# Kernel optimization log

Hardware: AMD Instinct MI355X
Metric: run time of the kernel (lower is better)

The kernel has to match this reference:

```python
import jax, jax.numpy as jnp
import numpy as np

N = 100000
E = 2000000
K = 3


def setup_inputs() -> dict:
    key = jax.random.key(0)
    ks = jax.random.split(key, 6)
    x = jax.random.normal(ks[0], (N, 1), jnp.float32)
    edge_index = jax.random.randint(ks[1], (2, E), 0, N, dtype=jnp.int64)
    W1 = jax.random.normal(ks[2], (K, 1, 32), jnp.float32) * 0.5
    b1 = jnp.zeros((32,), jnp.float32)
    W2 = jax.random.normal(ks[3], (K, 32, 32), jnp.float32) * (1.0 / np.sqrt(32.0))
    b2 = jnp.zeros((32,), jnp.float32)
    Wfc = jax.random.normal(ks[4], (32, 1), jnp.float32) * (1.0 / np.sqrt(32.0))
    bfc = jnp.zeros((1,), jnp.float32)
    return dict(x=x, edge_index=edge_index, W1=W1, b1=b1, W2=W2, b2=b2, Wfc=Wfc, bfc=bfc)


def _cheb_norm(edge_index, n):
    # PyG ChebConv.__norm__ with normalization='sym', lambda_max=2.0:
    # L = I - D^{-1/2} A D^{-1/2}; L_hat = (2/lmax)*L - I = -D^{-1/2} A D^{-1/2} (zero diag)
    src, dst = edge_index[0], edge_index[1]
    w = jnp.ones((edge_index.shape[1],), jnp.float32)
    deg = jax.ops.segment_sum(w, src, num_segments=n)
    dinv = jnp.where(deg > 0, jax.lax.rsqrt(jnp.maximum(deg, 1.0)), 0.0)
    norm = -dinv[src] * w * dinv[dst]
    return src, dst, norm


def _propagate(x, src, dst, norm, n):
    # y[i] = sum_{e: dst[e]=i} norm[e] * x[src[e]]  (gather-scatter SpMM)
    return jax.ops.segment_sum(norm[:, None] * x[src], dst, num_segments=n)


def _cheb_conv(x, src, dst, norm, W, b, n):
    Tx0 = x
    out = Tx0 @ W[0]
    Tx1 = _propagate(Tx0, src, dst, norm, n)
    out = out + Tx1 @ W[1]
    for k in range(2, W.shape[0]):  # small fixed K, structurally distinct weights
        Tx2 = 2.0 * _propagate(Tx1, src, dst, norm, n) - Tx0
        out = out + Tx2 @ W[k]
        Tx0, Tx1 = Tx1, Tx2
    return out + b


def reference(x, edge_index, W1, b1, W2, b2, Wfc, bfc):
    n = x.shape[0]
    src, dst, norm = _cheb_norm(edge_index, n)
    h = jax.nn.relu(_cheb_conv(x, src, dst, norm, W1, b1, n))
    h = jax.nn.relu(_cheb_conv(h, src, dst, norm, W2, b2, n))
    return h @ Wfc + bfc
```

## Files before the change

kernel.cpp:

```cpp
#include <hip/hip_runtime.h>
#include <hip/hip_fp16.h>


#define BS 256
#define NC 32
#define NRH 16
#define NRB 16
#define HB 1024
#define RCAP 6250

__global__ __launch_bounds__(HB) void k_hist32(const int* __restrict__ src,
                                               const int* __restrict__ dst,
                                               int* __restrict__ deg32,
                                               int* __restrict__ cnt32,
                                               int n, int E, int ce) {
    __shared__ int hcnt[RCAP];
    __shared__ int hdeg[RCAP];
    int b = blockIdx.x, c = b & (NC - 1), r = b >> 5;
    int t = threadIdx.x;
    const int R = (n + NRH - 1) / NRH;
    int lo = r * R, hi = min(lo + R, n), len = hi - lo;
    for (int q = t; q < len; q += HB) { hcnt[q] = 0; hdeg[q] = 0; }
    __syncthreads();
    int e0 = c * ce, e1 = min(e0 + ce, E);
    if (e0 < e1) {
        const int4* d4 = reinterpret_cast<const int4*>(dst + e0);
        const int4* s4 = reinterpret_cast<const int4*>(src + e0);
        int L4 = (e1 - e0) >> 2;
        for (int m = 0; m * 4 * HB < L4; ++m) {
            int4 dv[4], sv[4];
            bool ok[4];
            #pragma unroll
            for (int q = 0; q < 4; ++q) {
                int idx = t + (m * 4 + q) * HB;
                ok[q] = idx < L4;
                if (ok[q]) { dv[q] = d4[idx]; sv[q] = s4[idx]; }
            }
            #pragma unroll
            for (int q = 0; q < 4; ++q) if (ok[q]) {
                int d;
                d = dv[q].x; if (d >= lo && d < hi) atomicAdd(&hcnt[d - lo], 1);
                d = dv[q].y; if (d >= lo && d < hi) atomicAdd(&hcnt[d - lo], 1);
                d = dv[q].z; if (d >= lo && d < hi) atomicAdd(&hcnt[d - lo], 1);
                d = dv[q].w; if (d >= lo && d < hi) atomicAdd(&hcnt[d - lo], 1);
                d = sv[q].x; if (d >= lo && d < hi) atomicAdd(&hdeg[d - lo], 1);
                d = sv[q].y; if (d >= lo && d < hi) atomicAdd(&hdeg[d - lo], 1);
                d = sv[q].z; if (d >= lo && d < hi) atomicAdd(&hdeg[d - lo], 1);
                d = sv[q].w; if (d >= lo && d < hi) atomicAdd(&hdeg[d - lo], 1);
            }
        }
        for (int e = e0 + ((e1 - e0) & ~3) + t; e < e1; e += HB) {
            int d = dst[e];
            if (d >= lo && d < hi) atomicAdd(&hcnt[d - lo], 1);
            int s = src[e];
            if (s >= lo && s < hi) atomicAdd(&hdeg[s - lo], 1);
        }
    }
    __syncthreads();
    int base = c * n + lo;
    for (int q = t; q < len; q += HB) {
        cnt32[base + q] = hcnt[q];
        deg32[base + q] = hdeg[q];
    }
}

__global__ void k_dinv32(const int* __restrict__ deg32, const int* __restrict__ cnt32,
                         const float* __restrict__ x, float* __restrict__ dinv,
                         float* __restrict__ u, float* __restrict__ w,
                         int* __restrict__ cnt, int n) {
    int i = blockIdx.x * BS + threadIdx.x;
    if (i < n) {
        int d = 0, ci = 0;
        #pragma unroll
        for (int c = 0; c < NC; ++c) { d += deg32[c * n + i]; ci += cnt32[c * n + i]; }
        float df = (float)d;
        float dv = (d > 0) ? rsqrtf(fmaxf(df, 1.0f)) : 0.0f;
        dinv[i] = dv;
        u[i] = dv * x[i];
        w[i] = -dv * dv;
        cnt[i] = ci;
    }
}

__global__ void k_scan2A(const int* __restrict__ cnt, int* __restrict__ rowptr,
                         int* __restrict__ part, int n) {
    __shared__ int sh[BS];
    int t = threadIdx.x, i = blockIdx.x * BS + t;
    int v = (i < n) ? cnt[i] : 0;
    sh[t] = v; __syncthreads();
    int acc = v;
    for (int d = 1; d < BS; d <<= 1) {
        int add = (t >= d) ? sh[t - d] : 0;
        __syncthreads();
        acc += add; sh[t] = acc;
        __syncthreads();
    }
    if (i < n) rowptr[i] = acc - v;
    if (t == BS - 1) part[blockIdx.x] = acc;
}

__global__ void k_scanB(int* __restrict__ part, int nb) {
    __shared__ int sh[512];
    int t = threadIdx.x;
    int v = (t < nb) ? part[t] : 0;
    sh[t] = v; __syncthreads();
    int acc = v;
    for (int d = 1; d < 512; d <<= 1) {
        int add = (t >= d) ? sh[t - d] : 0;
        __syncthreads();
        acc += add; sh[t] = acc;
        __syncthreads();
    }
    if (t < nb) part[t] = acc - v;
}

__global__ void k_scan2C(int* __restrict__ rowptr, const int* __restrict__ part, int n, int E) {
    int i = blockIdx.x * BS + threadIdx.x;
    if (i < n) rowptr[i] += part[i >> 8];
    if (i == n) rowptr[n] = E;
}

__global__ void k_frag(const int* __restrict__ cnt32, const int* __restrict__ rowptr,
                       int* __restrict__ cur32, int n) {
    int i = blockIdx.x * BS + threadIdx.x;
    if (i < n) {
        int run = rowptr[i];
        #pragma unroll
        for (int c = 0; c < NC; ++c) {
            cur32[c * n + i] = run;
            run += cnt32[c * n + i];
        }
    }
}

__global__ __launch_bounds__(HB) void k_build32(const int* __restrict__ src,
                                                const int* __restrict__ dst,
                                                const int* __restrict__ cur32,
                                                int* __restrict__ colv,
                                                int n, int E, int ce) {
    __shared__ int lcur[RCAP];
    int b = blockIdx.x, r = b & (NRB - 1), c = b >> 4;
    int t = threadIdx.x;
    const int R = (n + NRB - 1) / NRB;
    int lo = r * R, hi = min(lo + R, n), len = hi - lo;
    int base = c * n + lo;
    for (int q = t; q < len; q += HB) lcur[q] = cur32[base + q];
    __syncthreads();
    int e0 = c * ce, e1 = min(e0 + ce, E);
    if (e0 < e1) {
        const int4* d4 = reinterpret_cast<const int4*>(dst + e0);
        const int4* s4 = reinterpret_cast<const int4*>(src + e0);
        int L4 = (e1 - e0) >> 2;
        for (int m = 0; m * 4 * HB < L4; ++m) {
            int4 dv[4], sv[4];
            bool ok[4];
            #pragma unroll
            for (int q = 0; q < 4; ++q) {
                int idx = t + (m * 4 + q) * HB;
                ok[q] = idx < L4;
                if (ok[q]) { dv[q] = d4[idx]; sv[q] = s4[idx]; }
            }
            #pragma unroll
            for (int q = 0; q < 4; ++q) if (ok[q]) {
                int d;
                d = dv[q].x; if (d >= lo && d < hi) { int p = atomicAdd(&lcur[d - lo], 1); colv[p] = sv[q].x; }
                d = dv[q].y; if (d >= lo && d < hi) { int p = atomicAdd(&lcur[d - lo], 1); colv[p] = sv[q].y; }
                d = dv[q].z; if (d >= lo && d < hi) { int p = atomicAdd(&lcur[d - lo], 1); colv[p] = sv[q].z; }
                d = dv[q].w; if (d >= lo && d < hi) { int p = atomicAdd(&lcur[d - lo], 1); colv[p] = sv[q].w; }
            }
        }
        for (int e = e0 + ((e1 - e0) & ~3) + t; e < e1; e += HB) {
            int d = dst[e];
            if (d >= lo && d < hi) { int p = atomicAdd(&lcur[d - lo], 1); colv[p] = src[e]; }
        }
    }
}

__global__ void k_prop_s(const int* __restrict__ rowptr, const int* __restrict__ colv,
                         const float* __restrict__ in, float* __restrict__ g,
                         float* __restrict__ vout, const float* __restrict__ w, int n) {
    int i = blockIdx.x * BS + threadIdx.x;
    if (i >= n) return;
    int b = rowptr[i], e = rowptr[i + 1];
    float s = 0.0f;
    int j = b;
    for (; j + 4 <= e; j += 4) {
        int s0 = colv[j], s1 = colv[j + 1], s2 = colv[j + 2], s3 = colv[j + 3];
        float a0 = in[s0], a1 = in[s1], a2 = in[s2], a3 = in[s3];
        s += (a0 + a1) + (a2 + a3);
    }
    for (; j < e; ++j) s += in[colv[j]];
    g[i] = s;
    if (vout) vout[i] = w[i] * s;
}

__global__ void k_layer1(const float* __restrict__ x, const float* __restrict__ g1,
                         const float* __restrict__ g2, const float* __restrict__ dinv,
                         const float* __restrict__ W1, const float* __restrict__ b1,
                         float* __restrict__ h, __half* __restrict__ hs16, int n) {
    int idx = blockIdx.x * BS + threadIdx.x;
    if (idx < n * 32) {
        int i = idx >> 5, f = idx & 31;
        float x0 = x[i], dv = dinv[i];
        float t1 = -dv * g1[i];
        float t2 = -2.0f * dv * g2[i] - x0;
        float v = x0 * W1[f] + t1 * W1[32 + f] + t2 * W1[64 + f] + b1[f];
        v = fmaxf(v, 0.0f);
        h[idx] = v;
        hs16[idx] = __float2half_rn(dv * v);
    }
}

__global__ void k_prop_vh(const int* __restrict__ rowptr, const int* __restrict__ colv,
                          const __half* __restrict__ in16, const float* __restrict__ wsc,
                          float* __restrict__ outf, __half* __restrict__ out16, int n) {
    int t = blockIdx.x * BS + threadIdx.x;
    int node = t >> 3;
    if (node >= n) return;
    int ln4 = (t & 7) << 2;
    int b = rowptr[node], e = rowptr[node + 1];
    float4 acc = make_float4(0.f, 0.f, 0.f, 0.f);
    int j = b;
    for (; j + 8 <= e; j += 8) {
        int sx[8];
        #pragma unroll
        for (int q = 0; q < 8; ++q) sx[q] = colv[j + q];
        float2 raw[8];
        #pragma unroll
        for (int q = 0; q < 8; ++q)
            raw[q] = *reinterpret_cast<const float2*>(in16 + (size_t)sx[q] * 32 + ln4);
        #pragma unroll
        for (int q = 0; q < 8; ++q) {
            __half2 p0 = *reinterpret_cast<__half2*>(&raw[q].x);
            __half2 p1 = *reinterpret_cast<__half2*>(&raw[q].y);
            float2 a = __half22float2(p0), c = __half22float2(p1);
            acc.x += a.x; acc.y += a.y; acc.z += c.x; acc.w += c.y;
        }
    }
    for (; j < e; ++j) {
        int s = colv[j];
        float2 raw = *reinterpret_cast<const float2*>(in16 + (size_t)s * 32 + ln4);
        __half2 p0 = *reinterpret_cast<__half2*>(&raw.x);
        __half2 p1 = *reinterpret_cast<__half2*>(&raw.y);
        float2 a = __half22float2(p0), c = __half22float2(p1);
        acc.x += a.x; acc.y += a.y; acc.z += c.x; acc.w += c.y;
    }
    *reinterpret_cast<float4*>(outf + (size_t)node * 32 + ln4) = acc;
    float wn = wsc[node];
    __half2 o0 = __floats2half2_rn(wn * acc.x, wn * acc.y);
    __half2 o1 = __floats2half2_rn(wn * acc.z, wn * acc.w);
    float2 packed;
    *reinterpret_cast<__half2*>(&packed.x) = o0;
    *reinterpret_cast<__half2*>(&packed.y) = o1;
    *reinterpret_cast<float2*>(out16 + (size_t)node * 32 + ln4) = packed;
}

__global__ __launch_bounds__(BS) void k_prop_fc(
    const int* __restrict__ rowptr, const int* __restrict__ colv,
    const __half* __restrict__ gA16s, const float* __restrict__ h,
    const float* __restrict__ gA, const float* __restrict__ dinv,
    const float* __restrict__ W2, const float* __restrict__ b2,
    const float* __restrict__ Wfc, const float* __restrict__ bfc,
    float* __restrict__ out, int n) {
    __shared__ float W2s[3 * 32 * 32];
    int tid = threadIdx.x;
    for (int q = tid; q < 3 * 32 * 32; q += BS) W2s[q] = W2[q];
    __syncthreads();
    int nd = tid >> 3, ln = tid & 7, ln4 = ln << 2;
    int i = blockIdx.x * 32 + nd;
    if (i >= n) return;
    float4 acc = make_float4(0.f, 0.f, 0.f, 0.f);
    int b = rowptr[i], e = rowptr[i + 1];
    int j = b;
    for (; j + 8 <= e; j += 8) {
        int sx[8];
        #pragma unroll
        for (int q = 0; q < 8; ++q) sx[q] = colv[j + q];
        float2 raw[8];
        #pragma unroll
        for (int q = 0; q < 8; ++q)
            raw[q] = *reinterpret_cast<const float2*>(gA16s + (size_t)sx[q] * 32 + ln4);
        #pragma unroll
        for (int q = 0; q < 8; ++q) {
            __half2 p0 = *reinterpret_cast<__half2*>(&raw[q].x);
            __half2 p1 = *reinterpret_cast<__half2*>(&raw[q].y);
            float2 a = __half22float2(p0), c = __half22float2(p1);
            acc.x += a.x; acc.y += a.y; acc.z += c.x; acc.w += c.y;
        }
    }
    for (; j < e; ++j) {
        int s = colv[j];
        float2 raw = *reinterpret_cast<const float2*>(gA16s + (size_t)s * 32 + ln4);
        __half2 p0 = *reinterpret_cast<__half2*>(&raw.x);
        __half2 p1 = *reinterpret_cast<__half2*>(&raw.y);
        float2 a = __half22float2(p0), c = __half22float2(p1);
        acc.x += a.x; acc.y += a.y; acc.z += c.x; acc.w += c.y;
    }
    float dv = dinv[i];
    float4 hv  = *reinterpret_cast<const float4*>(h  + (size_t)i * 32 + ln4);
    float4 gav = *reinterpret_cast<const float4*>(gA + (size_t)i * 32 + ln4);
    float hkv[4] = { hv.x, hv.y, hv.z, hv.w };
    float s1v[4] = { -dv * gav.x, -dv * gav.y, -dv * gav.z, -dv * gav.w };
    float s2v[4] = { -2.0f * dv * acc.x - hv.x, -2.0f * dv * acc.y - hv.y,
                     -2.0f * dv * acc.z - hv.z, -2.0f * dv * acc.w - hv.w };
    float a0 = b2[ln4 + 0], a1 = b2[ln4 + 1], a2 = b2[ln4 + 2], a3 = b2[ln4 + 3];
    #pragma unroll
    for (int k = 0; k < 32; ++k) {
        int srcLn = k >> 2;
        float hk  = __shfl(hkv[k & 3], srcLn, 8);
        float s1k = __shfl(s1v[k & 3], srcLn, 8);
        float s2k = __shfl(s2v[k & 3], srcLn, 8);
        const float* w0 = W2s + k * 32 + ln4;
        a0 += hk * w0[0] + s1k * w0[1024] + s2k * w0[2048];
        a1 += hk * w0[1] + s1k * w0[1025] + s2k * w0[2049];
        a2 += hk * w0[2] + s1k * w0[1026] + s2k * w0[2050];
        a3 += hk * w0[3] + s1k * w0[1027] + s2k * w0[2051];
    }
    float p = fmaxf(a0, 0.f) * Wfc[ln4 + 0] + fmaxf(a1, 0.f) * Wfc[ln4 + 1]
            + fmaxf(a2, 0.f) * Wfc[ln4 + 2] + fmaxf(a3, 0.f) * Wfc[ln4 + 3];
    #pragma unroll
    for (int m = 4; m >= 1; m >>= 1) p += __shfl_xor(p, m, 8);
    if (ln == 0) out[i] = p + bfc[0];
}

extern "C" void kernel_launch(void* const* d_in, const int* in_sizes, int n_in,
                              void* d_out, int out_size, void* d_ws, size_t ws_size,
                              hipStream_t stream) {
    const float* x   = (const float*)d_in[0];
    const int*   ei  = (const int*)d_in[1];
    const float* W1  = (const float*)d_in[2];
    const float* b1  = (const float*)d_in[3];
    const float* W2  = (const float*)d_in[4];
    const float* b2  = (const float*)d_in[5];
    const float* Wfc = (const float*)d_in[6];
    const float* bfc = (const float*)d_in[7];
    float* out = (float*)d_out;

    const int n = in_sizes[0];
    const int E = in_sizes[1] / 2;
    const int* src = ei;
    const int* dst = ei + E;
    const int ce = (((E + NC - 1) / NC) + 3) & ~3;

    int*   cnt    = (int*)d_ws;
    int*   rowptr = cnt + n;
    int*   part   = rowptr + n + 4;
    float* dinv   = (float*)(part + 512);
    float* u      = dinv + n;
    float* w      = u + n;
    float* g1     = w + n;
    float* v1     = g1 + n;
    float* g2     = v1 + n;
    int*   colv   = (int*)(g2 + n);
    float* h      = (float*)(colv + E);
    float* R2     = h + (size_t)32 * n;
    float* gA     = R2 + (size_t)32 * n;
    __half* hs16  = (__half*)R2;
    __half* gA16s = (__half*)(R2 + (size_t)16 * n);
    int*   cnt32  = (int*)h;
    int*   cur32  = (int*)R2;
    int*   deg32  = (int*)gA;

    const int NB = (n + BS - 1) / BS;

    k_hist32<<<NC * NRH, HB, 0, stream>>>(src, dst, deg32, cnt32, n, E, ce);
    k_dinv32<<<NB, BS, 0, stream>>>(deg32, cnt32, x, dinv, u, w, cnt, n);
    k_scan2A<<<NB, BS, 0, stream>>>(cnt, rowptr, part, n);
    k_scanB<<<1, 512, 0, stream>>>(part, NB);
    k_scan2C<<<NB + 1, BS, 0, stream>>>(rowptr, part, n, E);
    k_frag<<<NB, BS, 0, stream>>>(cnt32, rowptr, cur32, n);
    k_build32<<<NC * NRB, HB, 0, stream>>>(src, dst, cur32, colv, n, E, ce);

    k_prop_s<<<NB, BS, 0, stream>>>(rowptr, colv, u, g1, v1, w, n);
    k_prop_s<<<NB, BS, 0, stream>>>(rowptr, colv, v1, g2, nullptr, nullptr, n);
    k_layer1<<<(n * 32 + BS - 1) / BS, BS, 0, stream>>>(x, g1, g2, dinv, W1, b1, h, hs16, n);

    k_prop_vh<<<(n * 8 + BS - 1) / BS, BS, 0, stream>>>(rowptr, colv, hs16, w, gA, gA16s, n);
    k_prop_fc<<<(n + 31) / 32, BS, 0, stream>>>(rowptr, colv, gA16s, h, gA, dinv,
                                                W2, b2, Wfc, bfc, out, n);
}
```

Before: 271.8 us.

## Use 4 lanes per node with 16-byte gathers and drop fp32 gA buffer

Both SpMM propagation kernels now assign 4 lanes per node instead of 8, and each lane gathers 8 halves with one 16-byte load, which halves the number of gather instructions per edge. k_prop_vh no longer writes the fp32 aggregate gA. k_prop_fc instead rebuilds the Tx1 term from the fp16 scaled copy gA16s by dividing by dinv, which cuts a 32-float-per-node write and read. The cost is that Tx1 in layer 2 now carries fp16 rounding, and each thread holds more registers and does more of the dense 32x96 contraction.

```diff
diff --git a/kernel.cpp b/kernel.cpp
--- a/kernel.cpp
+++ b/kernel.cpp
@@ -213,113 +213,129 @@
 
 __global__ void k_prop_vh(const int* __restrict__ rowptr, const int* __restrict__ colv,
                           const __half* __restrict__ in16, const float* __restrict__ wsc,
-                          float* __restrict__ outf, __half* __restrict__ out16, int n) {
+                          __half* __restrict__ out16, int n) {
     int t = blockIdx.x * BS + threadIdx.x;
-    int node = t >> 3;
+    int node = t >> 2;
     if (node >= n) return;
-    int ln4 = (t & 7) << 2;
+    int ln8 = (t & 3) << 3;
     int b = rowptr[node], e = rowptr[node + 1];
-    float4 acc = make_float4(0.f, 0.f, 0.f, 0.f);
+    float acc[8] = {0.f, 0.f, 0.f, 0.f, 0.f, 0.f, 0.f, 0.f};
     int j = b;
     for (; j + 8 <= e; j += 8) {
         int sx[8];
         #pragma unroll
         for (int q = 0; q < 8; ++q) sx[q] = colv[j + q];
-        float2 raw[8];
+        float4 raw[8];
         #pragma unroll
         for (int q = 0; q < 8; ++q)
-            raw[q] = *reinterpret_cast<const float2*>(in16 + (size_t)sx[q] * 32 + ln4);
+            raw[q] = *reinterpret_cast<const float4*>(in16 + (size_t)sx[q] * 32 + ln8);
         #pragma unroll
         for (int q = 0; q < 8; ++q) {
-            __half2 p0 = *reinterpret_cast<__half2*>(&raw[q].x);
-            __half2 p1 = *reinterpret_cast<__half2*>(&raw[q].y);
-            float2 a = __half22float2(p0), c = __half22float2(p1);
-            acc.x += a.x; acc.y += a.y; acc.z += c.x; acc.w += c.y;
+            const __half2* hp = reinterpret_cast<const __half2*>(&raw[q]);
+            #pragma unroll
+            for (int d = 0; d < 4; ++d) {
+                float2 f = __half22float2(hp[d]);
+                acc[2 * d] += f.x; acc[2 * d + 1] += f.y;
+            }
         }
     }
     for (; j < e; ++j) {
         int s = colv[j];
-        float2 raw = *reinterpret_cast<const float2*>(in16 + (size_t)s * 32 + ln4);
-        __half2 p0 = *reinterpret_cast<__half2*>(&raw.x);
-        __half2 p1 = *reinterpret_cast<__half2*>(&raw.y);
-        float2 a = __half22float2(p0), c = __half22float2(p1);
-        acc.x += a.x; acc.y += a.y; acc.z += c.x; acc.w += c.y;
-    }
-    *reinterpret_cast<float4*>(outf + (size_t)node * 32 + ln4) = acc;
+        float4 raw = *reinterpret_cast<const float4*>(in16 + (size_t)s * 32 + ln8);
+        const __half2* hp = reinterpret_cast<const __half2*>(&raw);
+        #pragma unroll
+        for (int d = 0; d < 4; ++d) {
+            float2 f = __half22float2(hp[d]);
+            acc[2 * d] += f.x; acc[2 * d + 1] += f.y;
+        }
+    }
     float wn = wsc[node];
-    __half2 o0 = __floats2half2_rn(wn * acc.x, wn * acc.y);
-    __half2 o1 = __floats2half2_rn(wn * acc.z, wn * acc.w);
-    float2 packed;
-    *reinterpret_cast<__half2*>(&packed.x) = o0;
-    *reinterpret_cast<__half2*>(&packed.y) = o1;
-    *reinterpret_cast<float2*>(out16 + (size_t)node * 32 + ln4) = packed;
+    float4 pk;
+    __half2* op = reinterpret_cast<__half2*>(&pk);
+    #pragma unroll
+    for (int d = 0; d < 4; ++d)
+        op[d] = __floats2half2_rn(wn * acc[2 * d], wn * acc[2 * d + 1]);
+    *reinterpret_cast<float4*>(out16 + (size_t)node * 32 + ln8) = pk;
 }
 
 __global__ __launch_bounds__(BS) void k_prop_fc(
     const int* __restrict__ rowptr, const int* __restrict__ colv,
     const __half* __restrict__ gA16s, const float* __restrict__ h,
-    const float* __restrict__ gA, const float* __restrict__ dinv,
-    const float* __restrict__ W2, const float* __restrict__ b2,
-    const float* __restrict__ Wfc, const float* __restrict__ bfc,
-    float* __restrict__ out, int n) {
+    const float* __restrict__ dinv, const float* __restrict__ W2,
+    const float* __restrict__ b2, const float* __restrict__ Wfc,
+    const float* __restrict__ bfc, float* __restrict__ out, int n) {
     __shared__ float W2s[3 * 32 * 32];
     int tid = threadIdx.x;
     for (int q = tid; q < 3 * 32 * 32; q += BS) W2s[q] = W2[q];
     __syncthreads();
-    int nd = tid >> 3, ln = tid & 7, ln4 = ln << 2;
-    int i = blockIdx.x * 32 + nd;
+    int nd = tid >> 2, ln = tid & 3, ln8 = ln << 3;
+    int i = blockIdx.x * 64 + nd;
     if (i >= n) return;
-    float4 acc = make_float4(0.f, 0.f, 0.f, 0.f);
+    float acc[8] = {0.f, 0.f, 0.f, 0.f, 0.f, 0.f, 0.f, 0.f};
     int b = rowptr[i], e = rowptr[i + 1];
     int j = b;
     for (; j + 8 <= e; j += 8) {
         int sx[8];
         #pragma unroll
         for (int q = 0; q < 8; ++q) sx[q] = colv[j + q];
-        float2 raw[8];
+        float4 raw[8];
         #pragma unroll
         for (int q = 0; q < 8; ++q)
-            raw[q] = *reinterpret_cast<const float2*>(gA16s + (size_t)sx[q] * 32 + ln4);
+            raw[q] = *reinterpret_cast<const float4*>(gA16s + (size_t)sx[q] * 32 + ln8);
         #pragma unroll
         for (int q = 0; q < 8; ++q) {
-            __half2 p0 = *reinterpret_cast<__half2*>(&raw[q].x);
-            __half2 p1 = *reinterpret_cast<__half2*>(&raw[q].y);
-            float2 a = __half22float2(p0), c = __half22float2(p1);
-            acc.x += a.x; acc.y += a.y; acc.z += c.x; acc.w += c.y;
+            const __half2* hp = reinterpret_cast<const __half2*>(&raw[q]);
+            #pragma unroll
+            for (int d = 0; d < 4; ++d) {
+                float2 f = __half22float2(hp[d]);
+                acc[2 * d] += f.x; acc[2 * d + 1] += f.y;
+            }
         }
     }
     for (; j < e; ++j) {
         int s = colv[j];
-        float2 raw = *reinterpret_cast<const float2*>(gA16s + (size_t)s * 32 + ln4);
-        __half2 p0 = *reinterpret_cast<__half2*>(&raw.x);
-        __half2 p1 = *reinterpret_cast<__half2*>(&raw.y);
-        float2 a = __half22float2(p0), c = __half22float2(p1);
-        acc.x += a.x; acc.y += a.y; acc.z += c.x; acc.w += c.y;
+        float4 raw = *reinterpret_cast<const float4*>(gA16s + (size_t)s * 32 + ln8);
+        const __half2* hp = reinterpret_cast<const __half2*>(&raw);
+        #pragma unroll
+        for (int d = 0; d < 4; ++d) {
+            float2 f = __half22float2(hp[d]);
+            acc[2 * d] += f.x; acc[2 * d + 1] += f.y;
+        }
     }
     float dv = dinv[i];
-    float4 hv  = *reinterpret_cast<const float4*>(h  + (size_t)i * 32 + ln4);
-    float4 gav = *reinterpret_cast<const float4*>(gA + (size_t)i * 32 + ln4);
-    float hkv[4] = { hv.x, hv.y, hv.z, hv.w };
-    float s1v[4] = { -dv * gav.x, -dv * gav.y, -dv * gav.z, -dv * gav.w };
-    float s2v[4] = { -2.0f * dv * acc.x - hv.x, -2.0f * dv * acc.y - hv.y,
-                     -2.0f * dv * acc.z - hv.z, -2.0f * dv * acc.w - hv.w };
-    float a0 = b2[ln4 + 0], a1 = b2[ln4 + 1], a2 = b2[ln4 + 2], a3 = b2[ln4 + 3];
+    float rdv = (dv > 0.0f) ? (1.0f / dv) : 0.0f;
+    float4 gaw = *reinterpret_cast<const float4*>(gA16s + (size_t)i * 32 + ln8);
+    const __half2* gp = reinterpret_cast<const __half2*>(&gaw);
+    float4 hv0 = *reinterpret_cast<const float4*>(h + (size_t)i * 32 + ln8);
+    float4 hv1 = *reinterpret_cast<const float4*>(h + (size_t)i * 32 + ln8 + 4);
+    float hkv[8] = { hv0.x, hv0.y, hv0.z, hv0.w, hv1.x, hv1.y, hv1.z, hv1.w };
+    float s1v[8], s2v[8];
+    #pragma unroll
+    for (int d = 0; d < 4; ++d) {
+        float2 g = __half22float2(gp[d]);
+        s1v[2 * d] = g.x * rdv; s1v[2 * d + 1] = g.y * rdv;
+    }
+    #pragma unroll
+    for (int q = 0; q < 8; ++q) s2v[q] = -2.0f * dv * acc[q] - hkv[q];
+    float a[8];
+    #pragma unroll
+    for (int q = 0; q < 8; ++q) a[q] = b2[ln8 + q];
     #pragma unroll
     for (int k = 0; k < 32; ++k) {
-        int srcLn = k >> 2;
-        float hk  = __shfl(hkv[k & 3], srcLn, 8);
-        float s1k = __shfl(s1v[k & 3], srcLn, 8);
-        float s2k = __shfl(s2v[k & 3], srcLn, 8);
-        const float* w0 = W2s + k * 32 + ln4;
-        a0 += hk * w0[0] + s1k * w0[1024] + s2k * w0[2048];
-        a1 += hk * w0[1] + s1k * w0[1025] + s2k * w0[2049];
-        a2 += hk * w0[2] + s1k * w0[1026] + s2k * w0[2050];
-        a3 += hk * w0[3] + s1k * w0[1027] + s2k * w0[2051];
-    }
-    float p = fmaxf(a0, 0.f) * Wfc[ln4 + 0] + fmaxf(a1, 0.f) * Wfc[ln4 + 1]
-            + fmaxf(a2, 0.f) * Wfc[ln4 + 2] + fmaxf(a3, 0.f) * Wfc[ln4 + 3];
-    #pragma unroll
-    for (int m = 4; m >= 1; m >>= 1) p += __shfl_xor(p, m, 8);
+        int srcLn = k >> 3;
+        float hk  = __shfl(hkv[k & 7], srcLn, 4);
+        float s1k = __shfl(s1v[k & 7], srcLn, 4);
+        float s2k = __shfl(s2v[k & 7], srcLn, 4);
+        const float* w0 = W2s + k * 32 + ln8;
+        #pragma unroll
+        for (int q = 0; q < 8; ++q)
+            a[q] += hk * w0[q] + s1k * w0[1024 + q] + s2k * w0[2048 + q];
+    }
+    float p = 0.0f;
+    #pragma unroll
+    for (int q = 0; q < 8; ++q) p += fmaxf(a[q], 0.0f) * Wfc[ln8 + q];
+    p += __shfl_xor(p, 1, 4);
+    p += __shfl_xor(p, 2, 4);
     if (ln == 0) out[i] = p + bfc[0];
 }
 
@@ -354,12 +370,12 @@
     int*   colv   = (int*)(g2 + n);
     float* h      = (float*)(colv + E);
     float* R2     = h + (size_t)32 * n;
-    float* gA     = R2 + (size_t)32 * n;
+    float* R3     = R2 + (size_t)32 * n;
     __half* hs16  = (__half*)R2;
     __half* gA16s = (__half*)(R2 + (size_t)16 * n);
     int*   cnt32  = (int*)h;
     int*   cur32  = (int*)R2;
-    int*   deg32  = (int*)gA;
+    int*   deg32  = (int*)R3;
 
     const int NB = (n + BS - 1) / BS;
 
@@ -375,7 +391,7 @@
     k_prop_s<<<NB, BS, 0, stream>>>(rowptr, colv, v1, g2, nullptr, nullptr, n);
     k_layer1<<<(n * 32 + BS - 1) / BS, BS, 0, stream>>>(x, g1, g2, dinv, W1, b1, h, hs16, n);
 
-    k_prop_vh<<<(n * 8 + BS - 1) / BS, BS, 0, stream>>>(rowptr, colv, hs16, w, gA, gA16s, n);
-    k_prop_fc<<<(n + 31) / 32, BS, 0, stream>>>(rowptr, colv, gA16s, h, gA, dinv,
+    k_prop_vh<<<(n * 4 + BS - 1) / BS, BS, 0, stream>>>(rowptr, colv, hs16, w, gA16s, n);
+    k_prop_fc<<<(n + 63) / 64, BS, 0, stream>>>(rowptr, colv, gA16s, h, dinv,
                                                 W2, b2, Wfc, bfc, out, n);
 }
```

After: 269.6 us. About the same (-0.8%).
